# Performance work log

Measured on AMD Instinct MI355X. Metric: run time of the kernel, lower is better.

## Reference

```python
import jax, jax.numpy as jnp
import numpy as np

T, N, F, L, A = 4, 16, 6, 1024, 21  # genomes, tiles, frames, tile length, alphabet
K, U = 20, 256                      # profile width, number of profiles


def setup_inputs() -> dict:
    key = jax.random.key(0)
    k1, k2 = jax.random.split(key)
    X = jax.random.uniform(k1, (T, N, F, L, A), dtype=jnp.float32)
    Q = jnp.ones((A,), dtype=jnp.float32) / A  # uniform background distribution
    # P_logit ~ log(Q) + N(0, 4) as in _getRandomProfiles
    P_logit = (jnp.log(Q)[None, :, None]
               + 4.0 * jax.random.normal(k2, (K, A, U), dtype=jnp.float32))
    return {"X": X, "P_logit": P_logit, "Q": Q}


def reference(X, P_logit, Q):
    # SpecificProfile.call(X) -> (S, R, Z)
    Tb, Nb, Fb, Lb, Ab = X.shape
    k, _, units = P_logit.shape
    # getR: P = softmax(P_logit, axis=1); R = log(max(P / Q, epsilon))
    P = jax.nn.softmax(P_logit, axis=1)                    # [k, A, U]
    epsilon = jnp.mean(Q)                                   # exp(-log(1/mean(Q)))
    R = jnp.log(jnp.maximum(P / Q[None, :, None], epsilon))  # [k, A, U]
    # getZ: conv2d over (length, alphabet) spatial dims, VALID padding
    Xr = X.reshape(Tb * Nb * Fb, Lb, Ab, 1)                 # NHWC
    Kr = R[:, :, None, :]                                   # HWIO: [k, A, 1, U]
    Z = jax.lax.conv_general_dilated(
        Xr, Kr, window_strides=(1, 1), padding='VALID',
        dimension_numbers=('NHWC', 'HWIO', 'NHWC'))          # [TNF, L-k+1, 1, U]
    Z = Z.reshape(Tb, Nb, Fb, Lb - k + 1, units)            # [T, N, F, P, U]
    S = jnp.max(Z, axis=(2, 3))                             # [T, N, U]
    return S, R, Z
```

## Files before the change

### kernel.cpp

```cpp
#include <hip/hip_runtime.h>
#include <hip/hip_bf16.h>
#include <math.h>

#define T_ 4
#define N_ 16
#define F_ 6
#define L_ 1024
#define A_ 21
#define K_ 20
#define U_ 256
#define LOUT 1005
#define NIMG 384
#define SZ_S (T_*N_*U_)
#define SZ_R (K_*A_*U_)

#define XPR 24
#define XROWS 1056
#define NSTEP 15
#define XWCH 7

typedef __attribute__((ext_vector_type(8))) short short8;
typedef __attribute__((ext_vector_type(4))) float f32x4;
typedef __attribute__((ext_vector_type(4))) unsigned int uint4v;

__device__ __forceinline__ unsigned short f2bf(float f) {
  unsigned int u = __float_as_uint(f);
  u += 0x7FFFu + ((u >> 16) & 1u);
  return (unsigned short)(u >> 16);
}

__device__ __forceinline__ void atomicMaxF(float* addr, float val) {
  if (val >= 0.f) atomicMax((int*)addr, __float_as_int(val));
  else            atomicMin((unsigned int*)addr, __float_as_uint(val));
}

__device__ __forceinline__ void gload_lds16(const void* g, void* l) {
  __builtin_amdgcn_global_load_lds(
      (const __attribute__((address_space(1))) void*)g,
      (__attribute__((address_space(3))) void*)l, 16, 0, 0);
}

__global__ void xprep_kernel(const float* __restrict__ X,
                             const float* __restrict__ P_logit,
                             const float* __restrict__ Q,
                             float* __restrict__ out,
                             unsigned short* __restrict__ Rt,
                             unsigned int* __restrict__ Xp32) {
  int t = blockIdx.x * blockDim.x + threadIdx.x;
  if (t < SZ_S) out[t] = -INFINITY;

  if (t < K_ * U_) {
    int k = t / U_;
    int u = t - k * U_;
    const float* pl = P_logit + (size_t)k * A_ * U_ + u;
    float v[A_];
    float m = -INFINITY;
#pragma unroll
    for (int a = 0; a < A_; ++a) { v[a] = pl[(size_t)a * U_]; m = fmaxf(m, v[a]); }
    float s = 0.f;
#pragma unroll
    for (int a = 0; a < A_; ++a) { v[a] = expf(v[a] - m); s += v[a]; }
    float qs = 0.f;
#pragma unroll
    for (int a = 0; a < A_; ++a) qs += Q[a];
    float eps = qs * (1.0f / A_);
    float invs = 1.f / s;
    float* Rout = out + SZ_S;
    const int um = (u >> 1) & 3;
#pragma unroll
    for (int a = 0; a < XPR; ++a) {
      unsigned short bv = 0;
      if (a < A_) {
        float r = logf(fmaxf(v[a] * invs / Q[a], eps));
        Rout[(size_t)(k * A_ + a) * U_ + u] = r;
        bv = f2bf(r);
      }
      int sl = k * XPR + a;
      int w = sl & 31;
      int widx = (((w >> 3) ^ um) << 3) | (w & 7);
      Rt[(size_t)(sl >> 5) * (U_ * 32) + u * 32 + widx] = bv;
    }
  }

  if (t < NIMG * XROWS * 12) {
    int w  = t % 12;
    int rl = t / 12;
    int row = rl % XROWS;
    int n   = rl / XROWS;
    int c0 = w * 2;
    float v0 = 0.f, v1 = 0.f;
    if (row < L_) {
      const float* xr = X + ((size_t)n * L_ + row) * A_;
      if (c0 < A_)     v0 = xr[c0];
      if (c0 + 1 < A_) v1 = xr[c0 + 1];
    }
    unsigned int o = (unsigned int)f2bf(v0) | ((unsigned int)f2bf(v1) << 16);
    Xp32[(size_t)rl * 12 + w] = o;
  }
}

__global__ __launch_bounds__(256, 1) void conv_kernel(
    const unsigned short* __restrict__ Xp,
    const unsigned short* __restrict__ Rt,
    float* __restrict__ out) {
  __shared__ __align__(16) unsigned short lds_r[NSTEP * 4096];
  __shared__ __align__(16) unsigned short lds_xp[4][XWCH * 512];

  const int n  = blockIdx.z;
  const int u0 = blockIdx.x * 128;
  const int wid  = threadIdx.x >> 6;
  const int lane = threadIdx.x & 63;
  const int wl = wid >> 1;
  const int wu = wid & 1;

  const char* xsrc = (const char*)Xp +
      ((size_t)n * XROWS + wl * 128) * (XPR * 2);
  const char* rsrc = (const char*)Rt + (size_t)u0 * 64;
  char* xdst = (char*)&lds_xp[wid][0];

  for (int c = wid; c < NSTEP * 8; c += 4)
    gload_lds16(rsrc + (size_t)(c >> 3) * (U_ * 64) + (c & 7) * 1024 + lane * 16,
                (char*)lds_r + c * 1024);
#pragma unroll
  for (int c = 0; c < XWCH; ++c)
    gload_lds16(xsrc + c * 1024 + lane * 16, xdst + c * 1024);
  asm volatile("s_waitcnt vmcnt(0)" ::: "memory");
  __builtin_amdgcn_s_barrier();

  const int fl = lane & 15;
  const int fj = lane >> 4;
  const int rfo = (wu * 64 + fl) * 32 + ((fj ^ ((fl >> 1) & 3)) << 3);
  const unsigned short* xb =
      (const unsigned short*)xdst + fl * XPR + (fj << 3);
  const int ug = fj << 2;

  float* Z = out + SZ_S + SZ_R;
  float pmax[4][4];
#pragma unroll
  for (int ut = 0; ut < 4; ++ut)
#pragma unroll
    for (int r = 0; r < 4; ++r) pmax[ut][r] = -INFINITY;

  f32x4 accA[4][8], accB[4][8];
  uint4v xr[XWCH];

#define SGK(k) ((k)==1?0:(k)==2?1:(k)==4?2:(k)==5?3:(k)==7?4:(k)==9?5:   \
                (k)==10?6:(k)==12?7:-1)

#define ZERO(ACC)                                                            \
  {                                                                          \
    _Pragma("unroll")                                                        \
    for (int ut = 0; ut < 4; ++ut)                                           \
      _Pragma("unroll")                                                      \
      for (int lt = 0; lt < 8; ++lt)                                         \
        (ACC)[ut][lt] = (f32x4){0.f, 0.f, 0.f, 0.f};                         \
  }

#define KSTEP(K, ACC)                                                        \
  {                                                                          \
    short8 xfr[8], rfr[4];                                                   \
    const unsigned short* rb = lds_r + (K) * 4096 + rfo;                     \
    _Pragma("unroll")                                                        \
    for (int lt = 0; lt < 8; ++lt)                                           \
      xfr[lt] = *(const short8*)(xb + lt * (16 * XPR) + (K) * 32);           \
    _Pragma("unroll")                                                        \
    for (int ut = 0; ut < 4; ++ut)                                           \
      rfr[ut] = *(const short8*)(rb + ut * (16 * 32));                       \
    _Pragma("unroll")                                                        \
    for (int ut = 0; ut < 4; ++ut)                                           \
      _Pragma("unroll")                                                      \
      for (int lt = 0; lt < 8; ++lt)                                         \
        (ACC)[ut][lt] = __builtin_amdgcn_mfma_f32_16x16x32_bf16(             \
            rfr[ut], xfr[lt], (ACC)[ut][lt], 0, 0, 0);                       \
  }

#define STORE4(ACC, TT, LT)                                                  \
  {                                                                          \
    const int l = (TT) * 256 + wl * 128 + (LT) * 16 + fl;                    \
    float* zrow = Z + ((size_t)n * LOUT + l) * U_ + u0 + wu * 64 + ug;       \
    _Pragma("unroll")                                                        \
    for (int ut = 0; ut < 4; ++ut) {                                         \
      f32x4 v = (ACC)[ut][LT];                                               \
      *(f32x4*)(zrow + ut * 16) = v;                                         \
      _Pragma("unroll")                                                      \
      for (int r = 0; r < 4; ++r) pmax[ut][r] = fmaxf(pmax[ut][r], v[r]);    \
    }                                                                        \
  }

#define XLOADS(T1)                                                           \
  {                                                                          \
    const char* xs = xsrc + (size_t)(T1) * (256 * XPR * 2);                  \
    _Pragma("unroll")                                                        \
    for (int c = 0; c < XWCH; ++c)                                           \
      xr[c] = *(const uint4v*)(xs + c * 1024 + lane * 16);                   \
  }

#define XWRITE()                                                             \
  {                                                                          \
    _Pragma("unroll")                                                        \
    for (int c = 0; c < XWCH; ++c)                                           \
      *(uint4v*)(xdst + c * 1024 + lane * 16) = xr[c];                       \
  }

  ZERO(accA)
  XLOADS(1)
#pragma unroll
  for (int k = 0; k < NSTEP; ++k) KSTEP(k, accA)
  asm volatile("s_waitcnt vmcnt(0)" ::: "memory");
  XWRITE()

  ZERO(accB)
  XLOADS(2)
#pragma unroll
  for (int k = 0; k < NSTEP; ++k) {
    KSTEP(k, accB)
    if (SGK(k) >= 0) STORE4(accA, 0, SGK(k))
  }
  asm volatile("s_waitcnt vmcnt(32)" ::: "memory");
  XWRITE()

  ZERO(accA)
  XLOADS(3)
#pragma unroll
  for (int k = 0; k < NSTEP; ++k) {
    KSTEP(k, accA)
    if (SGK(k) >= 0) STORE4(accB, 1, SGK(k))
  }
  asm volatile("s_waitcnt vmcnt(32)" ::: "memory");
  XWRITE()

  ZERO(accB)
#pragma unroll
  for (int k = 0; k < NSTEP; ++k) {
    KSTEP(k, accB)
    if (SGK(k) >= 0) STORE4(accA, 2, SGK(k))
  }

#pragma unroll
  for (int lt = 0; lt < 8; ++lt) {
    const int l = 768 + wl * 128 + lt * 16 + fl;
    if (l < LOUT) {
      float* zrow = Z + ((size_t)n * LOUT + l) * U_ + u0 + wu * 64 + ug;
#pragma unroll
      for (int ut = 0; ut < 4; ++ut) {
        f32x4 v = accB[ut][lt];
        *(f32x4*)(zrow + ut * 16) = v;
#pragma unroll
        for (int r = 0; r < 4; ++r) pmax[ut][r] = fmaxf(pmax[ut][r], v[r]);
      }
    }
  }

#undef SGK
#undef ZERO
#undef KSTEP
#undef STORE4
#undef XLOADS
#undef XWRITE

#pragma unroll
  for (int off = 1; off < 16; off <<= 1)
#pragma unroll
    for (int ut = 0; ut < 4; ++ut)
#pragma unroll
      for (int r = 0; r < 4; ++r)
        pmax[ut][r] = fmaxf(pmax[ut][r], __shfl_xor(pmax[ut][r], off));

  if (fl == 0) {
    const int tn = n / F_;
    float* Sp = out + (size_t)tn * U_ + u0 + wu * 64 + ug;
#pragma unroll
    for (int ut = 0; ut < 4; ++ut)
#pragma unroll
      for (int r = 0; r < 4; ++r)
        atomicMaxF(Sp + ut * 16 + r, pmax[ut][r]);
  }
}

extern "C" void kernel_launch(void* const* d_in, const int* in_sizes, int n_in,
                              void* d_out, int out_size, void* d_ws, size_t ws_size,
                              hipStream_t stream) {
  const float* X       = (const float*)d_in[0];
  const float* P_logit = (const float*)d_in[1];
  const float* Q       = (const float*)d_in[2];
  float* out = (float*)d_out;

  unsigned short* Rt = (unsigned short*)d_ws;
  unsigned short* Xp = (unsigned short*)((char*)d_ws + 262144);

  int xthreads = NIMG * XROWS * 12;
  hipLaunchKernelGGL(xprep_kernel, dim3((xthreads + 255) / 256), dim3(256),
                     0, stream, X, P_logit, Q, out, Rt, (unsigned int*)Xp);
  dim3 grid(2, 1, NIMG);
  hipLaunchKernelGGL(conv_kernel, grid, dim3(256), 0, stream, Xp, Rt, out);
}
```

Before: 120.0 us.

## Fuse X bf16 conversion into conv kernel, dropping padded Xp staging buffer

The separate X-to-bf16 padding pass in the prep kernel is removed. The conv kernel now reads fp32 X directly from global memory, converts it to bf16 in registers, and writes it to LDS. This eliminates a full write and re-read of the intermediate buffer and shrinks the prep launch to just the R/S setup. In exchange, the conv kernel reads twice as many bytes per X tile (fp32 instead of bf16) and uses twice the staging registers. It also relies on unaligned 16-byte loads and on neighbouring-row data landing in pad columns, where the R weights are zero.

```diff
diff --git a/kernel.cpp b/kernel.cpp
--- a/kernel.cpp
+++ b/kernel.cpp
@@ -15,9 +15,9 @@
 #define SZ_R (K_*A_*U_)
 
 #define XPR 24
-#define XROWS 1056
 #define NSTEP 15
 #define XWCH 7
+#define XF_MAX ((size_t)NIMG * L_ * A_ - 8)
 
 typedef __attribute__((ext_vector_type(8))) short short8;
 typedef __attribute__((ext_vector_type(4))) float f32x4;
@@ -40,12 +40,10 @@
       (__attribute__((address_space(3))) void*)l, 16, 0, 0);
 }
 
-__global__ void xprep_kernel(const float* __restrict__ X,
-                             const float* __restrict__ P_logit,
+__global__ void xprep_kernel(const float* __restrict__ P_logit,
                              const float* __restrict__ Q,
                              float* __restrict__ out,
-                             unsigned short* __restrict__ Rt,
-                             unsigned int* __restrict__ Xp32) {
+                             unsigned short* __restrict__ Rt) {
   int t = blockIdx.x * blockDim.x + threadIdx.x;
   if (t < SZ_S) out[t] = -INFINITY;
 
@@ -81,26 +79,10 @@
       Rt[(size_t)(sl >> 5) * (U_ * 32) + u * 32 + widx] = bv;
     }
   }
-
-  if (t < NIMG * XROWS * 12) {
-    int w  = t % 12;
-    int rl = t / 12;
-    int row = rl % XROWS;
-    int n   = rl / XROWS;
-    int c0 = w * 2;
-    float v0 = 0.f, v1 = 0.f;
-    if (row < L_) {
-      const float* xr = X + ((size_t)n * L_ + row) * A_;
-      if (c0 < A_)     v0 = xr[c0];
-      if (c0 + 1 < A_) v1 = xr[c0 + 1];
-    }
-    unsigned int o = (unsigned int)f2bf(v0) | ((unsigned int)f2bf(v1) << 16);
-    Xp32[(size_t)rl * 12 + w] = o;
-  }
 }
 
 __global__ __launch_bounds__(256, 1) void conv_kernel(
-    const unsigned short* __restrict__ Xp,
+    const float* __restrict__ Xf,
     const unsigned short* __restrict__ Rt,
     float* __restrict__ out) {
   __shared__ __align__(16) unsigned short lds_r[NSTEP * 4096];
@@ -113,19 +95,8 @@
   const int wl = wid >> 1;
   const int wu = wid & 1;
 
-  const char* xsrc = (const char*)Xp +
-      ((size_t)n * XROWS + wl * 128) * (XPR * 2);
   const char* rsrc = (const char*)Rt + (size_t)u0 * 64;
   char* xdst = (char*)&lds_xp[wid][0];
-
-  for (int c = wid; c < NSTEP * 8; c += 4)
-    gload_lds16(rsrc + (size_t)(c >> 3) * (U_ * 64) + (c & 7) * 1024 + lane * 16,
-                (char*)lds_r + c * 1024);
-#pragma unroll
-  for (int c = 0; c < XWCH; ++c)
-    gload_lds16(xsrc + c * 1024 + lane * 16, xdst + c * 1024);
-  asm volatile("s_waitcnt vmcnt(0)" ::: "memory");
-  __builtin_amdgcn_s_barrier();
 
   const int fl = lane & 15;
   const int fj = lane >> 4;
@@ -142,7 +113,7 @@
     for (int r = 0; r < 4; ++r) pmax[ut][r] = -INFINITY;
 
   f32x4 accA[4][8], accB[4][8];
-  uint4v xr[XWCH];
+  uint4v xr[2 * XWCH];
 
 #define SGK(k) ((k)==1?0:(k)==2?1:(k)==4?2:(k)==5?3:(k)==7?4:(k)==9?5:   \
                 (k)==10?6:(k)==12?7:-1)
@@ -189,18 +160,41 @@
 
 #define XLOADS(T1)                                                           \
   {                                                                          \
-    const char* xs = xsrc + (size_t)(T1) * (256 * XPR * 2);                  \
-    _Pragma("unroll")                                                        \
-    for (int c = 0; c < XWCH; ++c)                                           \
-      xr[c] = *(const uint4v*)(xs + c * 1024 + lane * 16);                   \
+    const size_t base_row = (size_t)n * L_ + (T1) * 256 + wl * 128;          \
+    _Pragma("unroll")                                                        \
+    for (int c = 0; c < XWCH; ++c) {                                         \
+      int idx = c * 64 + lane;                                               \
+      int row = idx / 3, part = idx - row * 3;                               \
+      size_t f = (base_row + row) * A_ + part * 8;                           \
+      if (f > XF_MAX) f = XF_MAX;                                            \
+      xr[2 * c]     = *(const uint4v*)(Xf + f);                              \
+      xr[2 * c + 1] = *(const uint4v*)(Xf + f + 4);                          \
+    }                                                                        \
   }
 
 #define XWRITE()                                                             \
   {                                                                          \
     _Pragma("unroll")                                                        \
-    for (int c = 0; c < XWCH; ++c)                                           \
-      *(uint4v*)(xdst + c * 1024 + lane * 16) = xr[c];                       \
-  }
+    for (int c = 0; c < XWCH; ++c) {                                         \
+      uint4v o;                                                              \
+      _Pragma("unroll")                                                      \
+      for (int j = 0; j < 2; ++j) {                                          \
+        o[j]     = (unsigned int)f2bf(__uint_as_float(xr[2*c][2*j]))         \
+                 | ((unsigned int)f2bf(__uint_as_float(xr[2*c][2*j+1])) << 16);\
+        o[j + 2] = (unsigned int)f2bf(__uint_as_float(xr[2*c+1][2*j]))       \
+                 | ((unsigned int)f2bf(__uint_as_float(xr[2*c+1][2*j+1])) << 16);\
+      }                                                                      \
+      *(uint4v*)(xdst + c * 1024 + lane * 16) = o;                           \
+    }                                                                        \
+  }
+
+  for (int c = wid; c < NSTEP * 8; c += 4)
+    gload_lds16(rsrc + (size_t)(c >> 3) * (U_ * 64) + (c & 7) * 1024 + lane * 16,
+                (char*)lds_r + c * 1024);
+  XLOADS(0)
+  asm volatile("s_waitcnt vmcnt(0)" ::: "memory");
+  XWRITE()
+  __builtin_amdgcn_s_barrier();
 
   ZERO(accA)
   XLOADS(1)
@@ -286,11 +280,9 @@
   float* out = (float*)d_out;
 
   unsigned short* Rt = (unsigned short*)d_ws;
-  unsigned short* Xp = (unsigned short*)((char*)d_ws + 262144);
-
-  int xthreads = NIMG * XROWS * 12;
-  hipLaunchKernelGGL(xprep_kernel, dim3((xthreads + 255) / 256), dim3(256),
-                     0, stream, X, P_logit, Q, out, Rt, (unsigned int*)Xp);
+
+  hipLaunchKernelGGL(xprep_kernel, dim3(64), dim3(256), 0, stream,
+                     P_logit, Q, out, Rt);
   dim3 grid(2, 1, NIMG);
-  hipLaunchKernelGGL(conv_kernel, grid, dim3(256), 0, stream, Xp, Rt, out);
-}
+  hipLaunchKernelGGL(conv_kernel, grid, dim3(256), 0, stream, X, Rt, out);
+}
```

After: 120.1 us. About the same (+0.1%).
